# Kernel optimization log

Measured on AMD Instinct MI355X. Metric: run time of the kernel, lower is better.

The kernel has to match this reference:

```python
import jax, jax.numpy as jnp
import numpy as np

B, N, H, V = 8192, 12, 512, 256  # batch, n_columns, hidden_size, per-column vocab
LN_EPS = 1e-5


def setup_inputs() -> dict:
    key = jax.random.key(0)
    k0, k1, k2, k3 = jax.random.split(key, 4)
    return {
        "input_embedding": jax.random.normal(k0, (B, H), dtype=jnp.float32),
        "features": jax.random.randint(k1, (B, N), 0, V),  # one categorical id per column
        "emb_tables": jax.random.normal(k2, (N, V, H), dtype=jnp.float32) * 0.02,
        "ln_gamma": jnp.ones((2 * H,), dtype=jnp.float32),
        "ln_beta": jnp.zeros((2 * H,), dtype=jnp.float32),
        "pred_W": jax.random.normal(k3, (N, 2 * H, V), dtype=jnp.float32) * 0.02,
        "pred_b": jnp.zeros((N, V), dtype=jnp.float32),
    }


def reference(input_embedding, features, emb_tables, ln_gamma, ln_beta, pred_W, pred_b):
    n = features.shape[1]
    # per-column embedding lookup: emb[b, n] = emb_tables[n, features[b, n]]  -> [B, N, H]
    emb = emb_tables[jnp.arange(n)[None, :], features]
    # _make_masked_sums: triu(diagonal=1) mask summed over dim 1 == exclusive prefix sum
    # over the column axis: masked_sums[b, j] = sum_{i < j} emb[b, i]
    masked_sums = jnp.cumsum(emb, axis=1) - emb  # [B, N, H]
    ctx = jnp.broadcast_to(input_embedding[:, None, :], emb.shape)  # [B, N, H]
    x = jnp.concatenate([ctx, masked_sums], axis=-1)  # [B, N, 2H]
    # LayerNorm over last dim, then exact (erf) GELU as in torch nn.GELU default
    mu = jnp.mean(x, axis=-1, keepdims=True)
    var = jnp.mean(jnp.square(x - mu), axis=-1, keepdims=True)
    xn = (x - mu) * jax.lax.rsqrt(var + LN_EPS) * ln_gamma + ln_beta
    act = jax.nn.gelu(xn, approximate=False)
    # per-column predictor heads: logits[b, n, :] = act[b, n, :] @ pred_W[n] + pred_b[n]
    logits = jnp.einsum('bnh,nhv->bnv', act, pred_W) + pred_b
    return logits
```

## Files before the change

kernel.cpp:

```cpp
#include <hip/hip_runtime.h>
#include <stdint.h>

#define B_SZ 8192
#define N_F 12
#define H_DIM 512
#define K_DIM 1024
#define V_DIM 256

typedef __attribute__((ext_vector_type(8))) __bf16 bf16x8;
typedef __attribute__((ext_vector_type(4))) float f32x4;

__device__ inline float gelu_f(float x) {
  float t = 1.5957691216057308f * x * (1.0f + 0.044715f * x * x);
  return x / (1.0f + __expf(-t));
}

__device__ inline void gld_lds16(const void* g, void* l) {
  __builtin_amdgcn_global_load_lds(
      (const __attribute__((address_space(1))) void*)g,
      (__attribute__((address_space(3))) void*)l, 16, 0, 0);
}

__global__ __launch_bounds__(256, 8) void k_prep(
    const float* __restrict__ ie, const int* __restrict__ feat,
    const float* __restrict__ tab, const float* __restrict__ gam,
    const float* __restrict__ bet, __bf16* __restrict__ act2,
    float* __restrict__ stats) {
  const int lane = threadIdx.x & 63;
  const int b = blockIdx.x * 4 + (threadIdx.x >> 6);

  const float* cb = ie + (size_t)b * H_DIM + lane * 8;
  float4 c0 = *(const float4*)cb;
  float4 c1 = *(const float4*)(cb + 4);
  float s = c0.x + c0.y + c0.z + c0.w + c1.x + c1.y + c1.z + c1.w;
  float q = c0.x * c0.x + c0.y * c0.y + c0.z * c0.z + c0.w * c0.w +
            c1.x * c1.x + c1.y * c1.y + c1.z * c1.z + c1.w * c1.w;
#pragma unroll
  for (int o = 1; o < 64; o <<= 1) {
    s += __shfl_xor(s, o, 64);
    q += __shfl_xor(q, o, 64);
  }
  const float S1 = s, Q1 = q;

  const float4 g0 = *(const float4*)(gam + H_DIM + lane * 8);
  const float4 g1 = *(const float4*)(gam + H_DIM + lane * 8 + 4);
  const float4 e0 = *(const float4*)(bet + H_DIM + lane * 8);
  const float4 e1 = *(const float4*)(bet + H_DIM + lane * 8 + 4);

  float r[8];
#pragma unroll
  for (int i = 0; i < 8; ++i) r[i] = 0.f;

  const int sw = (lane & ~7) | ((lane & 7) ^ (b & 7));
  __bf16* arow = act2 + (size_t)b * H_DIM + sw * 8;

  for (int n = 0; n < N_F; ++n) {
    s = 0.f; q = 0.f;
#pragma unroll
    for (int i = 0; i < 8; ++i) { s += r[i]; q += r[i] * r[i]; }
#pragma unroll
    for (int o = 1; o < 64; o <<= 1) {
      s += __shfl_xor(s, o, 64);
      q += __shfl_xor(q, o, 64);
    }
    const float mean = (S1 + s) * (1.0f / 1024.0f);
    const float var = (Q1 + q) * (1.0f / 1024.0f) - mean * mean;
    const float rs = rsqrtf(var + 1e-5f);
    if (lane == 0)
      *(float2*)(stats + ((size_t)b * N_F + n) * 2) = make_float2(mean, rs);

    bf16x8 pk;
    pk[0] = (__bf16)gelu_f((r[0] - mean) * rs * g0.x + e0.x);
    pk[1] = (__bf16)gelu_f((r[1] - mean) * rs * g0.y + e0.y);
    pk[2] = (__bf16)gelu_f((r[2] - mean) * rs * g0.z + e0.z);
    pk[3] = (__bf16)gelu_f((r[3] - mean) * rs * g0.w + e0.w);
    pk[4] = (__bf16)gelu_f((r[4] - mean) * rs * g1.x + e1.x);
    pk[5] = (__bf16)gelu_f((r[5] - mean) * rs * g1.y + e1.y);
    pk[6] = (__bf16)gelu_f((r[6] - mean) * rs * g1.z + e1.z);
    pk[7] = (__bf16)gelu_f((r[7] - mean) * rs * g1.w + e1.w);
    *(bf16x8*)(arow + (size_t)n * B_SZ * H_DIM) = pk;

    if (n < N_F - 1) {
      const int f = feat[b * N_F + n];
      const float* tr = tab + ((size_t)n * V_DIM + f) * H_DIM + lane * 8;
      const float4 t0 = *(const float4*)tr;
      const float4 t1 = *(const float4*)(tr + 4);
      r[0] += t0.x; r[1] += t0.y; r[2] += t0.z; r[3] += t0.w;
      r[4] += t1.x; r[5] += t1.y; r[6] += t1.z; r[7] += t1.w;
    }
  }
}

__global__ __launch_bounds__(256) void k_wt(const float* __restrict__ W,
                                            __bf16* __restrict__ Wt) {
  __shared__ float tile[32][33];
  const int bid = blockIdx.x;
  const int n = bid >> 8;
  const int rem = bid & 255;
  const int kt = rem >> 3, vt = rem & 7;
  const int tx = threadIdx.x & 31, ty = threadIdx.x >> 5;
  const float* src = W + (size_t)n * K_DIM * V_DIM;
#pragma unroll
  for (int i = 0; i < 4; ++i) {
    const int k = kt * 32 + ty + i * 8;
    tile[ty + i * 8][tx] = src[(size_t)k * V_DIM + vt * 32 + tx];
  }
  __syncthreads();
  __bf16* dst = Wt + (size_t)n * V_DIM * K_DIM;
  const int t = threadIdx.x;
  if (t < 128) {
    const int v_l = t >> 2, c_l = t & 3;
    const int v = vt * 32 + v_l;
    bf16x8 pk;
#pragma unroll
    for (int e = 0; e < 8; ++e) pk[e] = (__bf16)tile[c_l * 8 + e][v_l];
    const int gc = kt * 4 + c_l;
    const int swc = (gc & ~7) | ((gc & 7) ^ (v & 7));
    *(bf16x8*)(dst + (size_t)v * K_DIM + swc * 8) = pk;
  }
}

__global__ __launch_bounds__(512, 4) void k_gemm(
    const float* __restrict__ ie, const __bf16* __restrict__ act2,
    const __bf16* __restrict__ Wt, const float* __restrict__ stats,
    const float* __restrict__ gam, const float* __restrict__ bet,
    const float* __restrict__ bias, float* __restrict__ out) {
  constexpr int BM = 128, BN = 256, BK = 64;
  __shared__ __align__(16) __bf16 As[BM * BK];
  __shared__ __align__(16) __bf16 Ws[BN * BK];
  __shared__ float muL[BM], rsL[BM];

  const int n = blockIdx.y;
  const int b0 = blockIdx.x * BM;
  const int t = threadIdx.x;
  const int lane = t & 63;
  const int w = t >> 6;
  const int wm = w & 1;
  const int wn = w >> 1;
  const int l15 = lane & 15;
  const int lq = lane >> 4;

  if (t < 2 * BM) {
    const int r = t >> 1, which = t & 1;
    const float v = stats[((size_t)(b0 + r) * N_F + n) * 2 + which];
    if (which == 0) muL[r] = v; else rsL[r] = v;
  }

  f32x4 acc[4][4];
#pragma unroll
  for (int i = 0; i < 4; ++i)
#pragma unroll
    for (int j = 0; j < 4; ++j) acc[i][j] = (f32x4){0.f, 0.f, 0.f, 0.f};

  const __bf16* act2n = act2 + (size_t)n * B_SZ * H_DIM;
  const __bf16* Wtn = Wt + (size_t)n * V_DIM * K_DIM;

  const int o8 = t & 7;
  const int rA = t >> 3;
  const int lr8 = lane >> 3;
  const int lo8 = lane & 7;

  for (int kt = 0; kt < 16; ++kt) {
    const int k0 = kt * BK;
    __syncthreads();
#pragma unroll
    for (int p = 0; p < 4; ++p) {
      const int v0 = w * 32 + p * 8;
      gld_lds16(Wtn + (size_t)(v0 + lr8) * K_DIM + k0 + lo8 * 8, Ws + v0 * BK);
    }
    if (k0 < H_DIM) {
      const int kk = k0 + o8 * 8;
      const float4 gg0 = *(const float4*)(gam + kk);
      const float4 gg1 = *(const float4*)(gam + kk + 4);
      const float4 bt0 = *(const float4*)(bet + kk);
      const float4 bt1 = *(const float4*)(bet + kk + 4);
      const int swo = (o8 ^ (rA & 7)) * 8;
#pragma unroll
      for (int half = 0; half < 2; ++half) {
        const int r = rA + half * 64;
        const float* cp = ie + (size_t)(b0 + r) * H_DIM + kk;
        const float4 x0 = *(const float4*)cp;
        const float4 x1 = *(const float4*)(cp + 4);
        const float mu = muL[r], rs = rsL[r];
        bf16x8 pk;
        pk[0] = (__bf16)gelu_f((x0.x - mu) * rs * gg0.x + bt0.x);
        pk[1] = (__bf16)gelu_f((x0.y - mu) * rs * gg0.y + bt0.y);
        pk[2] = (__bf16)gelu_f((x0.z - mu) * rs * gg0.z + bt0.z);
        pk[3] = (__bf16)gelu_f((x0.w - mu) * rs * gg0.w + bt0.w);
        pk[4] = (__bf16)gelu_f((x1.x - mu) * rs * gg1.x + bt1.x);
        pk[5] = (__bf16)gelu_f((x1.y - mu) * rs * gg1.y + bt1.y);
        pk[6] = (__bf16)gelu_f((x1.z - mu) * rs * gg1.z + bt1.z);
        pk[7] = (__bf16)gelu_f((x1.w - mu) * rs * gg1.w + bt1.w);
        *(bf16x8*)(As + r * BK + swo) = pk;
      }
    } else {
#pragma unroll
      for (int p = 0; p < 2; ++p) {
        const int r0 = w * 16 + p * 8;
        gld_lds16(act2n + (size_t)(b0 + r0 + lr8) * H_DIM + (k0 - H_DIM) + lo8 * 8,
                  As + r0 * BK);
      }
    }
    __syncthreads();
#pragma unroll
    for (int ks = 0; ks < 2; ++ks) {
      const int cs = ks * 4 + lq;
      bf16x8 af[4], bb[4];
#pragma unroll
      for (int i = 0; i < 4; ++i) {
        const int row = wm * 64 + i * 16 + l15;
        af[i] = *(const bf16x8*)(As + row * BK + ((cs ^ (row & 7)) << 3));
      }
#pragma unroll
      for (int j = 0; j < 4; ++j) {
        const int row = wn * 64 + j * 16 + l15;
        bb[j] = *(const bf16x8*)(Ws + row * BK + ((cs ^ (row & 7)) << 3));
      }
#pragma unroll
      for (int i = 0; i < 4; ++i)
#pragma unroll
        for (int j = 0; j < 4; ++j)
          acc[i][j] =
              __builtin_amdgcn_mfma_f32_16x16x32_bf16(af[i], bb[j], acc[i][j], 0, 0, 0);
    }
  }

#pragma unroll
  for (int j = 0; j < 4; ++j) {
    const int v = wn * 64 + j * 16 + l15;
    const float bv = bias[n * V_DIM + v];
#pragma unroll
    for (int i = 0; i < 4; ++i) {
      const int rb = wm * 64 + i * 16 + lq * 4;
#pragma unroll
      for (int r = 0; r < 4; ++r) {
        out[((size_t)(b0 + rb + r) * N_F + n) * V_DIM + v] = acc[i][j][r] + bv;
      }
    }
  }
}

extern "C" void kernel_launch(void* const* d_in, const int* in_sizes, int n_in,
                              void* d_out, int out_size, void* d_ws, size_t ws_size,
                              hipStream_t stream) {
  const float* ie = (const float*)d_in[0];
  const int* feat = (const int*)d_in[1];
  const float* tab = (const float*)d_in[2];
  const float* gam = (const float*)d_in[3];
  const float* bet = (const float*)d_in[4];
  const float* predW = (const float*)d_in[5];
  const float* predb = (const float*)d_in[6];
  float* out = (float*)d_out;

  char* ws = (char*)d_ws;
  __bf16* act2 = (__bf16*)ws;
  float* stats = (float*)(ws + 100663296);
  __bf16* Wt = (__bf16*)(ws + 100663296 + 786432);

  hipLaunchKernelGGL(k_prep, dim3(B_SZ / 4), dim3(256), 0, stream, ie, feat,
                     tab, gam, bet, act2, stats);
  hipLaunchKernelGGL(k_wt, dim3(3072), dim3(256), 0, stream, predW, Wt);
  hipLaunchKernelGGL(k_gemm, dim3(B_SZ / 128, N_F), dim3(512), 0, stream, ie,
                     act2, Wt, stats, gam, bet, predb, out);
}
```

Baseline: 280.3 us.

## Precompute full bf16 activations in prep kernel, simplify GEMM A-loading

The context half of each activation row (LayerNorm plus GELU of the input embedding) is now computed in the prep kernel and stored as bf16 alongside the masked-sum half, so the GEMM loads its A tile for all K steps with async global-to-LDS copies. This removes the per-block stats staging and the in-GEMM GELU work on the first half of K. The trade is double the activation buffer written and read from memory (about 200 MB instead of 100 MB) and more ALU work in prep. The embedding-table load is also hoisted earlier in the loop to overlap with the GELU compute, and prep occupancy hint is lowered.

```diff
diff --git a/kernel.cpp b/kernel.cpp
--- a/kernel.cpp
+++ b/kernel.cpp
@@ -21,11 +21,10 @@
       (__attribute__((address_space(3))) void*)l, 16, 0, 0);
 }
 
-__global__ __launch_bounds__(256, 8) void k_prep(
+__global__ __launch_bounds__(256, 4) void k_prep(
     const float* __restrict__ ie, const int* __restrict__ feat,
     const float* __restrict__ tab, const float* __restrict__ gam,
-    const float* __restrict__ bet, __bf16* __restrict__ act2,
-    float* __restrict__ stats) {
+    const float* __restrict__ bet, __bf16* __restrict__ act2) {
   const int lane = threadIdx.x & 63;
   const int b = blockIdx.x * 4 + (threadIdx.x >> 6);
 
@@ -42,6 +41,10 @@
   }
   const float S1 = s, Q1 = q;
 
+  const float4 gl0 = *(const float4*)(gam + lane * 8);
+  const float4 gl1 = *(const float4*)(gam + lane * 8 + 4);
+  const float4 el0 = *(const float4*)(bet + lane * 8);
+  const float4 el1 = *(const float4*)(bet + lane * 8 + 4);
   const float4 g0 = *(const float4*)(gam + H_DIM + lane * 8);
   const float4 g1 = *(const float4*)(gam + H_DIM + lane * 8 + 4);
   const float4 e0 = *(const float4*)(bet + H_DIM + lane * 8);
@@ -52,7 +55,7 @@
   for (int i = 0; i < 8; ++i) r[i] = 0.f;
 
   const int sw = (lane & ~7) | ((lane & 7) ^ (b & 7));
-  __bf16* arow = act2 + (size_t)b * H_DIM + sw * 8;
+  __bf16* arow = act2 + (size_t)b * K_DIM + sw * 8;
 
   for (int n = 0; n < N_F; ++n) {
     s = 0.f; q = 0.f;
@@ -66,8 +69,26 @@
     const float mean = (S1 + s) * (1.0f / 1024.0f);
     const float var = (Q1 + q) * (1.0f / 1024.0f) - mean * mean;
     const float rs = rsqrtf(var + 1e-5f);
-    if (lane == 0)
-      *(float2*)(stats + ((size_t)b * N_F + n) * 2) = make_float2(mean, rs);
+
+    float4 t0, t1;
+    const bool have = (n < N_F - 1);
+    if (have) {
+      const int f = feat[b * N_F + n];
+      const float* tr = tab + ((size_t)n * V_DIM + f) * H_DIM + lane * 8;
+      t0 = *(const float4*)tr;
+      t1 = *(const float4*)(tr + 4);
+    }
+
+    bf16x8 pc;
+    pc[0] = (__bf16)gelu_f((c0.x - mean) * rs * gl0.x + el0.x);
+    pc[1] = (__bf16)gelu_f((c0.y - mean) * rs * gl0.y + el0.y);
+    pc[2] = (__bf16)gelu_f((c0.z - mean) * rs * gl0.z + el0.z);
+    pc[3] = (__bf16)gelu_f((c0.w - mean) * rs * gl0.w + el0.w);
+    pc[4] = (__bf16)gelu_f((c1.x - mean) * rs * gl1.x + el1.x);
+    pc[5] = (__bf16)gelu_f((c1.y - mean) * rs * gl1.y + el1.y);
+    pc[6] = (__bf16)gelu_f((c1.z - mean) * rs * gl1.z + el1.z);
+    pc[7] = (__bf16)gelu_f((c1.w - mean) * rs * gl1.w + el1.w);
+    *(bf16x8*)(arow + (size_t)n * B_SZ * K_DIM) = pc;
 
     bf16x8 pk;
     pk[0] = (__bf16)gelu_f((r[0] - mean) * rs * g0.x + e0.x);
@@ -78,13 +99,9 @@
     pk[5] = (__bf16)gelu_f((r[5] - mean) * rs * g1.y + e1.y);
     pk[6] = (__bf16)gelu_f((r[6] - mean) * rs * g1.z + e1.z);
     pk[7] = (__bf16)gelu_f((r[7] - mean) * rs * g1.w + e1.w);
-    *(bf16x8*)(arow + (size_t)n * B_SZ * H_DIM) = pk;
-
-    if (n < N_F - 1) {
-      const int f = feat[b * N_F + n];
-      const float* tr = tab + ((size_t)n * V_DIM + f) * H_DIM + lane * 8;
-      const float4 t0 = *(const float4*)tr;
-      const float4 t1 = *(const float4*)(tr + 4);
+    *(bf16x8*)(arow + (size_t)n * B_SZ * K_DIM + H_DIM) = pk;
+
+    if (have) {
       r[0] += t0.x; r[1] += t0.y; r[2] += t0.z; r[3] += t0.w;
       r[4] += t1.x; r[5] += t1.y; r[6] += t1.z; r[7] += t1.w;
     }
@@ -121,14 +138,11 @@
 }
 
 __global__ __launch_bounds__(512, 4) void k_gemm(
-    const float* __restrict__ ie, const __bf16* __restrict__ act2,
-    const __bf16* __restrict__ Wt, const float* __restrict__ stats,
-    const float* __restrict__ gam, const float* __restrict__ bet,
+    const __bf16* __restrict__ act2, const __bf16* __restrict__ Wt,
     const float* __restrict__ bias, float* __restrict__ out) {
   constexpr int BM = 128, BN = 256, BK = 64;
   __shared__ __align__(16) __bf16 As[BM * BK];
   __shared__ __align__(16) __bf16 Ws[BN * BK];
-  __shared__ float muL[BM], rsL[BM];
 
   const int n = blockIdx.y;
   const int b0 = blockIdx.x * BM;
@@ -140,23 +154,15 @@
   const int l15 = lane & 15;
   const int lq = lane >> 4;
 
-  if (t < 2 * BM) {
-    const int r = t >> 1, which = t & 1;
-    const float v = stats[((size_t)(b0 + r) * N_F + n) * 2 + which];
-    if (which == 0) muL[r] = v; else rsL[r] = v;
-  }
-
   f32x4 acc[4][4];
 #pragma unroll
   for (int i = 0; i < 4; ++i)
 #pragma unroll
     for (int j = 0; j < 4; ++j) acc[i][j] = (f32x4){0.f, 0.f, 0.f, 0.f};
 
-  const __bf16* act2n = act2 + (size_t)n * B_SZ * H_DIM;
+  const __bf16* act2n = act2 + (size_t)n * B_SZ * K_DIM;
   const __bf16* Wtn = Wt + (size_t)n * V_DIM * K_DIM;
 
-  const int o8 = t & 7;
-  const int rA = t >> 3;
   const int lr8 = lane >> 3;
   const int lo8 = lane & 7;
 
@@ -168,38 +174,11 @@
       const int v0 = w * 32 + p * 8;
       gld_lds16(Wtn + (size_t)(v0 + lr8) * K_DIM + k0 + lo8 * 8, Ws + v0 * BK);
     }
-    if (k0 < H_DIM) {
-      const int kk = k0 + o8 * 8;
-      const float4 gg0 = *(const float4*)(gam + kk);
-      const float4 gg1 = *(const float4*)(gam + kk + 4);
-      const float4 bt0 = *(const float4*)(bet + kk);
-      const float4 bt1 = *(const float4*)(bet + kk + 4);
-      const int swo = (o8 ^ (rA & 7)) * 8;
-#pragma unroll
-      for (int half = 0; half < 2; ++half) {
-        const int r = rA + half * 64;
-        const float* cp = ie + (size_t)(b0 + r) * H_DIM + kk;
-        const float4 x0 = *(const float4*)cp;
-        const float4 x1 = *(const float4*)(cp + 4);
-        const float mu = muL[r], rs = rsL[r];
-        bf16x8 pk;
-        pk[0] = (__bf16)gelu_f((x0.x - mu) * rs * gg0.x + bt0.x);
-        pk[1] = (__bf16)gelu_f((x0.y - mu) * rs * gg0.y + bt0.y);
-        pk[2] = (__bf16)gelu_f((x0.z - mu) * rs * gg0.z + bt0.z);
-        pk[3] = (__bf16)gelu_f((x0.w - mu) * rs * gg0.w + bt0.w);
-        pk[4] = (__bf16)gelu_f((x1.x - mu) * rs * gg1.x + bt1.x);
-        pk[5] = (__bf16)gelu_f((x1.y - mu) * rs * gg1.y + bt1.y);
-        pk[6] = (__bf16)gelu_f((x1.z - mu) * rs * gg1.z + bt1.z);
-        pk[7] = (__bf16)gelu_f((x1.w - mu) * rs * gg1.w + bt1.w);
-        *(bf16x8*)(As + r * BK + swo) = pk;
-      }
-    } else {
-#pragma unroll
-      for (int p = 0; p < 2; ++p) {
-        const int r0 = w * 16 + p * 8;
-        gld_lds16(act2n + (size_t)(b0 + r0 + lr8) * H_DIM + (k0 - H_DIM) + lo8 * 8,
-                  As + r0 * BK);
-      }
+#pragma unroll
+    for (int p = 0; p < 2; ++p) {
+      const int r0 = w * 16 + p * 8;
+      gld_lds16(act2n + (size_t)(b0 + r0 + lr8) * K_DIM + k0 + lo8 * 8,
+                As + r0 * BK);
     }
     __syncthreads();
 #pragma unroll
@@ -254,12 +233,11 @@
 
   char* ws = (char*)d_ws;
   __bf16* act2 = (__bf16*)ws;
-  float* stats = (float*)(ws + 100663296);
-  __bf16* Wt = (__bf16*)(ws + 100663296 + 786432);
+  __bf16* Wt = (__bf16*)(ws + 201326592);
 
   hipLaunchKernelGGL(k_prep, dim3(B_SZ / 4), dim3(256), 0, stream, ie, feat,
-                     tab, gam, bet, act2, stats);
+                     tab, gam, bet, act2);
   hipLaunchKernelGGL(k_wt, dim3(3072), dim3(256), 0, stream, predW, Wt);
-  hipLaunchKernelGGL(k_gemm, dim3(B_SZ / 128, N_F), dim3(512), 0, stream, ie,
-                     act2, Wt, stats, gam, bet, predb, out);
-}
+  hipLaunchKernelGGL(k_gemm, dim3(B_SZ / 128, N_F), dim3(512), 0, stream,
+                     act2, Wt, predb, out);
+}
```

After: 286.1 us. 1.02x slower.

## Double-buffer GEMM tiles and precompute context activations in registers

Applied to the files above, without the earlier changes.

The GEMM kernel now keeps two LDS buffers for the A and W tiles and prefetches the next K tile while MFMAs run on the current one, so each iteration needs one barrier instead of two. The context half of the A operand (LayerNorm+GELU of input_embedding) is computed up front for all 8 K tiles and held in 16 bf16x8 registers per thread, then stored to LDS each step. In the prep kernel, the embedding-row load is issued before the GELU packing so its latency is hidden. The costs are higher LDS use and register pressure, with launch bounds lowered to 2 blocks per SM to accommodate them.

```diff
diff --git a/kernel.cpp b/kernel.cpp
--- a/kernel.cpp
+++ b/kernel.cpp
@@ -68,6 +68,15 @@
     const float rs = rsqrtf(var + 1e-5f);
     if (lane == 0)
       *(float2*)(stats + ((size_t)b * N_F + n) * 2) = make_float2(mean, rs);
+
+    float4 t0, t1;
+    const bool have = (n < N_F - 1);
+    if (have) {
+      const int f = feat[b * N_F + n];
+      const float* tr = tab + ((size_t)n * V_DIM + f) * H_DIM + lane * 8;
+      t0 = *(const float4*)tr;
+      t1 = *(const float4*)(tr + 4);
+    }
 
     bf16x8 pk;
     pk[0] = (__bf16)gelu_f((r[0] - mean) * rs * g0.x + e0.x);
@@ -80,11 +89,7 @@
     pk[7] = (__bf16)gelu_f((r[7] - mean) * rs * g1.w + e1.w);
     *(bf16x8*)(arow + (size_t)n * B_SZ * H_DIM) = pk;
 
-    if (n < N_F - 1) {
-      const int f = feat[b * N_F + n];
-      const float* tr = tab + ((size_t)n * V_DIM + f) * H_DIM + lane * 8;
-      const float4 t0 = *(const float4*)tr;
-      const float4 t1 = *(const float4*)(tr + 4);
+    if (have) {
       r[0] += t0.x; r[1] += t0.y; r[2] += t0.z; r[3] += t0.w;
       r[4] += t1.x; r[5] += t1.y; r[6] += t1.z; r[7] += t1.w;
     }
@@ -120,15 +125,14 @@
   }
 }
 
-__global__ __launch_bounds__(512, 4) void k_gemm(
+__global__ __launch_bounds__(512, 2) void k_gemm(
     const float* __restrict__ ie, const __bf16* __restrict__ act2,
     const __bf16* __restrict__ Wt, const float* __restrict__ stats,
     const float* __restrict__ gam, const float* __restrict__ bet,
     const float* __restrict__ bias, float* __restrict__ out) {
   constexpr int BM = 128, BN = 256, BK = 64;
-  __shared__ __align__(16) __bf16 As[BM * BK];
-  __shared__ __align__(16) __bf16 Ws[BN * BK];
-  __shared__ float muL[BM], rsL[BM];
+  __shared__ __align__(16) __bf16 As[2][BM * BK];
+  __shared__ __align__(16) __bf16 Ws[2][BN * BK];
 
   const int n = blockIdx.y;
   const int b0 = blockIdx.x * BM;
@@ -139,69 +143,90 @@
   const int wn = w >> 1;
   const int l15 = lane & 15;
   const int lq = lane >> 4;
-
-  if (t < 2 * BM) {
-    const int r = t >> 1, which = t & 1;
-    const float v = stats[((size_t)(b0 + r) * N_F + n) * 2 + which];
-    if (which == 0) muL[r] = v; else rsL[r] = v;
-  }
-
-  f32x4 acc[4][4];
-#pragma unroll
-  for (int i = 0; i < 4; ++i)
-#pragma unroll
-    for (int j = 0; j < 4; ++j) acc[i][j] = (f32x4){0.f, 0.f, 0.f, 0.f};
+  const int lr8 = lane >> 3;
+  const int lo8 = lane & 7;
 
   const __bf16* act2n = act2 + (size_t)n * B_SZ * H_DIM;
   const __bf16* Wtn = Wt + (size_t)n * V_DIM * K_DIM;
 
-  const int o8 = t & 7;
-  const int rA = t >> 3;
-  const int lr8 = lane >> 3;
-  const int lo8 = lane & 7;
-
-  for (int kt = 0; kt < 16; ++kt) {
-    const int k0 = kt * BK;
-    __syncthreads();
+  {
+    const int k0 = 0;
 #pragma unroll
     for (int p = 0; p < 4; ++p) {
       const int v0 = w * 32 + p * 8;
-      gld_lds16(Wtn + (size_t)(v0 + lr8) * K_DIM + k0 + lo8 * 8, Ws + v0 * BK);
-    }
-    if (k0 < H_DIM) {
-      const int kk = k0 + o8 * 8;
-      const float4 gg0 = *(const float4*)(gam + kk);
-      const float4 gg1 = *(const float4*)(gam + kk + 4);
-      const float4 bt0 = *(const float4*)(bet + kk);
-      const float4 bt1 = *(const float4*)(bet + kk + 4);
-      const int swo = (o8 ^ (rA & 7)) * 8;
-#pragma unroll
-      for (int half = 0; half < 2; ++half) {
-        const int r = rA + half * 64;
-        const float* cp = ie + (size_t)(b0 + r) * H_DIM + kk;
-        const float4 x0 = *(const float4*)cp;
-        const float4 x1 = *(const float4*)(cp + 4);
-        const float mu = muL[r], rs = rsL[r];
+      gld_lds16(Wtn + (size_t)(v0 + lr8) * K_DIM + k0 + lo8 * 8,
+                &Ws[0][v0 * BK]);
+    }
+  }
+
+  const int pr = t >> 2;
+  const int pm = t & 3;
+  bf16x8 ctx[16];
+  {
+    const float2 st = *(const float2*)(stats + ((size_t)(b0 + pr) * N_F + n) * 2);
+    const float mu = st.x, rs = st.y;
+    const float* ierow = ie + (size_t)(b0 + pr) * H_DIM;
+#pragma unroll
+    for (int k8 = 0; k8 < 8; ++k8) {
+#pragma unroll
+      for (int h = 0; h < 2; ++h) {
+        const int col = k8 * 64 + pm * 16 + h * 8;
+        const float4 x0 = *(const float4*)(ierow + col);
+        const float4 x1 = *(const float4*)(ierow + col + 4);
+        const float4 gg0 = *(const float4*)(gam + col);
+        const float4 gg1 = *(const float4*)(gam + col + 4);
+        const float4 bb0 = *(const float4*)(bet + col);
+        const float4 bb1 = *(const float4*)(bet + col + 4);
         bf16x8 pk;
-        pk[0] = (__bf16)gelu_f((x0.x - mu) * rs * gg0.x + bt0.x);
-        pk[1] = (__bf16)gelu_f((x0.y - mu) * rs * gg0.y + bt0.y);
-        pk[2] = (__bf16)gelu_f((x0.z - mu) * rs * gg0.z + bt0.z);
-        pk[3] = (__bf16)gelu_f((x0.w - mu) * rs * gg0.w + bt0.w);
-        pk[4] = (__bf16)gelu_f((x1.x - mu) * rs * gg1.x + bt1.x);
-        pk[5] = (__bf16)gelu_f((x1.y - mu) * rs * gg1.y + bt1.y);
-        pk[6] = (__bf16)gelu_f((x1.z - mu) * rs * gg1.z + bt1.z);
-        pk[7] = (__bf16)gelu_f((x1.w - mu) * rs * gg1.w + bt1.w);
-        *(bf16x8*)(As + r * BK + swo) = pk;
-      }
-    } else {
-#pragma unroll
-      for (int p = 0; p < 2; ++p) {
-        const int r0 = w * 16 + p * 8;
-        gld_lds16(act2n + (size_t)(b0 + r0 + lr8) * H_DIM + (k0 - H_DIM) + lo8 * 8,
-                  As + r0 * BK);
-      }
-    }
-    __syncthreads();
+        pk[0] = (__bf16)gelu_f((x0.x - mu) * rs * gg0.x + bb0.x);
+        pk[1] = (__bf16)gelu_f((x0.y - mu) * rs * gg0.y + bb0.y);
+        pk[2] = (__bf16)gelu_f((x0.z - mu) * rs * gg0.z + bb0.z);
+        pk[3] = (__bf16)gelu_f((x0.w - mu) * rs * gg0.w + bb0.w);
+        pk[4] = (__bf16)gelu_f((x1.x - mu) * rs * gg1.x + bb1.x);
+        pk[5] = (__bf16)gelu_f((x1.y - mu) * rs * gg1.y + bb1.y);
+        pk[6] = (__bf16)gelu_f((x1.z - mu) * rs * gg1.z + bb1.z);
+        pk[7] = (__bf16)gelu_f((x1.w - mu) * rs * gg1.w + bb1.w);
+        ctx[k8 * 2 + h] = pk;
+      }
+    }
+  }
+
+  const int sA0 = pr * BK + (((pm * 2) ^ (pr & 7)) << 3);
+  const int sA1 = pr * BK + (((pm * 2 + 1) ^ (pr & 7)) << 3);
+
+  f32x4 acc[4][4];
+#pragma unroll
+  for (int i = 0; i < 4; ++i)
+#pragma unroll
+    for (int j = 0; j < 4; ++j) acc[i][j] = (f32x4){0.f, 0.f, 0.f, 0.f};
+
+  *(bf16x8*)(&As[0][sA0]) = ctx[0];
+  *(bf16x8*)(&As[0][sA1]) = ctx[1];
+  __syncthreads();
+
+  int cur = 0;
+#pragma unroll
+  for (int kt = 0; kt < 16; ++kt) {
+    if (kt < 15) {
+      const int k0 = (kt + 1) * BK;
+#pragma unroll
+      for (int p = 0; p < 4; ++p) {
+        const int v0 = w * 32 + p * 8;
+        gld_lds16(Wtn + (size_t)(v0 + lr8) * K_DIM + k0 + lo8 * 8,
+                  &Ws[cur ^ 1][v0 * BK]);
+      }
+      if (kt + 1 < 8) {
+        *(bf16x8*)(&As[cur ^ 1][sA0]) = ctx[(kt + 1) * 2];
+        *(bf16x8*)(&As[cur ^ 1][sA1]) = ctx[(kt + 1) * 2 + 1];
+      } else {
+#pragma unroll
+        for (int p = 0; p < 2; ++p) {
+          const int r0 = w * 16 + p * 8;
+          gld_lds16(act2n + (size_t)(b0 + r0 + lr8) * H_DIM + (k0 - H_DIM) + lo8 * 8,
+                    &As[cur ^ 1][r0 * BK]);
+        }
+      }
+    }
 #pragma unroll
     for (int ks = 0; ks < 2; ++ks) {
       const int cs = ks * 4 + lq;
@@ -209,20 +234,22 @@
 #pragma unroll
       for (int i = 0; i < 4; ++i) {
         const int row = wm * 64 + i * 16 + l15;
-        af[i] = *(const bf16x8*)(As + row * BK + ((cs ^ (row & 7)) << 3));
+        af[i] = *(const bf16x8*)(&As[cur][row * BK + ((cs ^ (row & 7)) << 3)]);
       }
 #pragma unroll
       for (int j = 0; j < 4; ++j) {
         const int row = wn * 64 + j * 16 + l15;
-        bb[j] = *(const bf16x8*)(Ws + row * BK + ((cs ^ (row & 7)) << 3));
+        bb[j] = *(const bf16x8*)(&Ws[cur][row * BK + ((cs ^ (row & 7)) << 3)]);
       }
 #pragma unroll
       for (int i = 0; i < 4; ++i)
 #pragma unroll
         for (int j = 0; j < 4; ++j)
-          acc[i][j] =
-              __builtin_amdgcn_mfma_f32_16x16x32_bf16(af[i], bb[j], acc[i][j], 0, 0, 0);
-    }
+          acc[i][j] = __builtin_amdgcn_mfma_f32_16x16x32_bf16(af[i], bb[j],
+                                                              acc[i][j], 0, 0, 0);
+    }
+    __syncthreads();
+    cur ^= 1;
   }
 
 #pragma unroll
```

After: 275.4 us. About the same (-1.8%).
